# Kernel optimization log

Hardware: AMD Instinct MI355X
Metric: run time of the kernel (lower is better)

Reference implementation:

```python
import jax, jax.numpy as jnp
import numpy as np

N, E, D, R = 8192, 131072, 128, 32
SIZES = (3, 5, 7)  # per-degree component counts (2l+1)
LN_EPS = 1e-5


def setup_inputs() -> dict:
    key = jax.random.key(0)
    ks = jax.random.split(key, 20)
    rn = lambda k, shape, s=1.0: jax.random.normal(k, shape, jnp.float32) * s
    inp = {
        'X0': rn(ks[0], (N, SIZES[0], D)),
        'X1': rn(ks[1], (N, SIZES[1], D)),
        'X2': rn(ks[2], (N, SIZES[2], D)),
        't_ij': rn(ks[3], (E, D)),
        'r0': rn(ks[4], (E, SIZES[0])),
        'r1': rn(ks[5], (E, SIZES[1])),
        'r2': rn(ks[6], (E, SIZES[2])),
        'edge_index': jax.random.randint(ks[7], (2, E), 0, N, dtype=jnp.int32),
        # params
        'W_vq': rn(ks[8], (D, R), D ** -0.5),
        'W_vk0': rn(ks[9], (D, R), D ** -0.5),
        'W_vk1': rn(ks[10], (D, R), D ** -0.5),
        'W_vk2': rn(ks[11], (D, R), D ** -0.5),
        'ln_g': jnp.ones((R,), jnp.float32),
        'ln_b': jnp.zeros((R,), jnp.float32),
        'W_w': rn(ks[12], (R, D), R ** -0.5),
        'b_w': jnp.zeros((D,), jnp.float32),
        'W_t1': rn(ks[13], (D, D), D ** -0.5),
        'b_t1': jnp.zeros((D,), jnp.float32),
        'W_t2': rn(ks[14], (D, D), D ** -0.5),
        'b_t2': jnp.zeros((D,), jnp.float32),
    }
    return inp


def _vec_rej(x, r):
    # x: [E, L, R], r: [E, L]; dot over component dim (L), keepdim, subtract projection
    r = r[..., None]
    dot = jnp.sum(x * r, axis=1, keepdims=True)  # [E, 1, R]
    return x - dot * r


def reference(X0, X1, X2, t_ij, r0, r1, r2, edge_index,
              W_vq, W_vk0, W_vk1, W_vk2, ln_g, ln_b, W_w, b_w,
              W_t1, b_t1, W_t2, b_t2):
    n_j, n_i = edge_index[0], edge_index[1]
    X_ls = jnp.concatenate([X0, X1, X2], axis=1)                 # [N, 15, D]
    eq_i = jnp.einsum('nld,dr->nlr', X_ls, W_vq)[n_i]            # [E, 15, R]
    ek = jnp.concatenate([
        jnp.einsum('nld,dr->nlr', X0, W_vk0),
        jnp.einsum('nld,dr->nlr', X1, W_vk1),
        jnp.einsum('nld,dr->nlr', X2, W_vk2)], axis=1)
    ek_j = ek[n_j]                                               # [E, 15, R]
    # per-degree vector rejection (vec_rej=True)
    qs, ksl, off = [], [], 0
    for r in (r0, r1, r2):
        s = r.shape[1]
        qs.append(_vec_rej(eq_i[:, off:off + s], r))
        ksl.append(_vec_rej(ek_j[:, off:off + s], -r))
        off += s
    eq_i = jnp.concatenate(qs, axis=1)
    ek_j = jnp.concatenate(ksl, axis=1)
    w_ij = jnp.sum(eq_i * ek_j, axis=1)                          # [E, R]
    # mlp_w = LayerNorm + Linear
    mu = jnp.mean(w_ij, axis=-1, keepdims=True)
    var = jnp.var(w_ij, axis=-1, keepdims=True)
    wn = (w_ij - mu) * jax.lax.rsqrt(var + LN_EPS) * ln_g + ln_b
    dw = wn @ W_w + b_w                                          # [E, D]
    # mlp_t = Linear -> silu -> Linear, then outer activation
    t = jax.nn.silu(t_ij @ W_t1 + b_t1) @ W_t2 + b_t2            # [E, D]
    return dw * jax.nn.silu(t)
```

## Files before the change

kernel.cpp:

```cpp
#include <hip/hip_runtime.h>
#include <hip/hip_bf16.h>

#define N_NODES 8192
#define N_EDGES 131072
#define LN_EPS  1e-5f

typedef __attribute__((ext_vector_type(8))) short bf16x8;
typedef __attribute__((ext_vector_type(4))) short bf16x4;
typedef __attribute__((ext_vector_type(4))) float f32x4;

__device__ __forceinline__ float silu_f(float x) {
    return x * __builtin_amdgcn_rcpf(1.0f + __expf(-x));
}

__device__ __forceinline__ unsigned short f2bf(float x) {
    union { float f; unsigned int u; } v; v.f = x;
    unsigned int r = v.u + 0x7FFFu + ((v.u >> 16) & 1u);
    return (unsigned short)(r >> 16);
}
__device__ __forceinline__ float bf2f(unsigned short u) {
    union { float f; unsigned int x; } v; v.x = ((unsigned int)u) << 16;
    return v.f;
}
__device__ __forceinline__ unsigned int pk2(float a, float b) {
    float2 t; t.x = a; t.y = b;
    union { __hip_bfloat162 h; unsigned int u; } v;
    v.h = __float22bfloat162_rn(t);
    return v.u;
}
__device__ __forceinline__ bf16x8 pack8(float4 u, float4 v) {
    union { bf16x8 b; unsigned int w[4]; } o;
    o.w[0] = pk2(u.x, u.y); o.w[1] = pk2(u.z, u.w);
    o.w[2] = pk2(v.x, v.y); o.w[3] = pk2(v.z, v.w);
    return o.b;
}
__device__ __forceinline__ bf16x4 pack4(float a, float b, float c, float d) {
    union { bf16x4 v; unsigned int u[2]; } o;
    o.u[0] = pk2(a, b); o.u[1] = pk2(c, d);
    return o.v;
}
__device__ __forceinline__ f32x4 mfma16(bf16x8 a, bf16x8 b, f32x4 c) {
    return __builtin_amdgcn_mfma_f32_16x16x32_bf16(a, b, c, 0, 0, 0);
}
#if __has_builtin(__builtin_amdgcn_mfma_f32_16x16x16bf16_1k)
__device__ __forceinline__ f32x4 mfma_k16(bf16x4 a, bf16x4 b, f32x4 c) {
    return __builtin_amdgcn_mfma_f32_16x16x16bf16_1k(a, b, c, 0, 0, 0);
}
#else
__device__ __forceinline__ f32x4 mfma_k16(bf16x4 a, bf16x4 b, f32x4 c) {
    f32x4 d;
    asm("v_mfma_f32_16x16x16_bf16 %0, %1, %2, %3"
        : "=v"(d) : "v"(a), "v"(b), "v"(c));
    return d;
}
#endif

__global__ __launch_bounds__(256) void prep_kernel(
    const float* __restrict__ W_w, const float* __restrict__ W_t1,
    const float* __restrict__ W_t2, const float* __restrict__ Wvq,
    const float* __restrict__ Wvk0, const float* __restrict__ Wvk1,
    const float* __restrict__ Wvk2,
    unsigned short* __restrict__ Wtw, unsigned short* __restrict__ Wt1b,
    unsigned short* __restrict__ Wt2b, unsigned short* __restrict__ Wqt,
    unsigned short* __restrict__ Wk0t, unsigned short* __restrict__ Wk1t,
    unsigned short* __restrict__ Wk2t)
{
    int i = blockIdx.x * 256 + threadIdx.x;
    if (i < 16384) {
        int n = i >> 7, k = i & 127;
        Wt1b[i] = f2bf(W_t1[k * 128 + n]);
        Wt2b[i] = f2bf(W_t2[k * 128 + n]);
    }
    if (i < 4096) {
        { int n = i >> 5, k = i & 31; Wtw[i] = f2bf(W_w[k * 128 + n]); }
        int r = i >> 7, d = i & 127;
        Wqt[i]  = f2bf(Wvq [d * 32 + r]);
        Wk0t[i] = f2bf(Wvk0[d * 32 + r]);
        Wk1t[i] = f2bf(Wvk1[d * 32 + r]);
        Wk2t[i] = f2bf(Wvk2[d * 32 + r]);
    }
}

template<int S, int LOFF>
__device__ __forceinline__ void proj_body(
    const float* __restrict__ X, const unsigned short* __restrict__ Wqt,
    const unsigned short* __restrict__ Wkt,
    unsigned short* __restrict__ eq, unsigned short* __restrict__ ek,
    int row0)
{
    const int tid  = threadIdx.x;
    const int lane = tid & 63;
    const int wv   = tid >> 6;
    const int l15  = lane & 15;
    const int lk   = lane >> 4;
    const int xrow = row0 + wv * 16 + l15;

    bf16x8 xf[4];
    #pragma unroll
    for (int kt = 0; kt < 4; ++kt) {
        const float* p = X + (size_t)xrow * 128 + kt * 32 + lk * 8;
        xf[kt] = pack8(*(const float4*)p, *(const float4*)(p + 4));
    }

    f32x4 qa[2], ka[2];
    #pragma unroll
    for (int h = 0; h < 2; ++h) {
        qa[h] = (f32x4){0.f, 0.f, 0.f, 0.f};
        ka[h] = (f32x4){0.f, 0.f, 0.f, 0.f};
    }
    #pragma unroll
    for (int kt = 0; kt < 4; ++kt) {
        #pragma unroll
        for (int h = 0; h < 2; ++h) {
            bf16x8 wq = *(const bf16x8*)&Wqt[(h * 16 + l15) * 128 + kt * 32 + lk * 8];
            bf16x8 wk = *(const bf16x8*)&Wkt[(h * 16 + l15) * 128 + kt * 32 + lk * 8];
            qa[h] = mfma16(wq, xf[kt], qa[h]);
            ka[h] = mfma16(wk, xf[kt], ka[h]);
        }
    }

    const int n = xrow / S;
    const int l = xrow % S + LOFF;
    const size_t base = (size_t)n * 512 + l;
    #pragma unroll
    for (int h = 0; h < 2; ++h) {
        #pragma unroll
        for (int j = 0; j < 4; ++j) {
            const int r = h * 16 + lk * 4 + j;
            eq[base + r * 16] = f2bf(qa[h][j]);
            ek[base + r * 16] = f2bf(ka[h][j]);
        }
    }
}

__global__ __launch_bounds__(256) void proj_kernel(
    const float* __restrict__ X0, const float* __restrict__ X1,
    const float* __restrict__ X2,
    const unsigned short* __restrict__ Wqt,
    const unsigned short* __restrict__ Wk0t,
    const unsigned short* __restrict__ Wk1t,
    const unsigned short* __restrict__ Wk2t,
    unsigned short* __restrict__ eq, unsigned short* __restrict__ ek)
{
    const int b = blockIdx.x;
    if (b < 384)
        proj_body<3, 0>(X0, Wqt, Wk0t, eq, ek, b * 64);
    else if (b < 1024)
        proj_body<5, 3>(X1, Wqt, Wk1t, eq, ek, (b - 384) * 64);
    else
        proj_body<7, 8>(X2, Wqt, Wk2t, eq, ek, (b - 1024) * 64);
}

__device__ __forceinline__ float edge_w(
    bf16x8 q0, bf16x8 q1, bf16x8 k0, bf16x8 k1, const float* rv)
{
    float qv[15], kv[15];
    #pragma unroll
    for (int l = 0; l < 8; ++l) {
        qv[l] = bf2f((unsigned short)q0[l]);
        kv[l] = bf2f((unsigned short)k0[l]);
    }
    #pragma unroll
    for (int l = 8; l < 15; ++l) {
        qv[l] = bf2f((unsigned short)q1[l - 8]);
        kv[l] = bf2f((unsigned short)k1[l - 8]);
    }
    float qk = 0.f;
    #pragma unroll
    for (int l = 0; l < 15; ++l) qk = fmaf(qv[l], kv[l], qk);
    float c0 = 2.f, c1 = 2.f, c2 = 2.f;
    #pragma unroll
    for (int l = 0; l < 3; ++l)  c0 -= rv[l] * rv[l];
    #pragma unroll
    for (int l = 3; l < 8; ++l)  c1 -= rv[l] * rv[l];
    #pragma unroll
    for (int l = 8; l < 15; ++l) c2 -= rv[l] * rv[l];
    float dq0 = 0.f, dk0 = 0.f, dq1 = 0.f, dk1 = 0.f, dq2 = 0.f, dk2 = 0.f;
    #pragma unroll
    for (int l = 0; l < 3; ++l)  { dq0 = fmaf(qv[l], rv[l], dq0); dk0 = fmaf(kv[l], rv[l], dk0); }
    #pragma unroll
    for (int l = 3; l < 8; ++l)  { dq1 = fmaf(qv[l], rv[l], dq1); dk1 = fmaf(kv[l], rv[l], dk1); }
    #pragma unroll
    for (int l = 8; l < 15; ++l) { dq2 = fmaf(qv[l], rv[l], dq2); dk2 = fmaf(kv[l], rv[l], dk2); }
    return qk - dq0 * dk0 * c0 - dq1 * dk1 * c1 - dq2 * dk2 * c2;
}

__global__ __launch_bounds__(256) void wn_kernel(
    const unsigned short* __restrict__ eq, const unsigned short* __restrict__ ek,
    const float* __restrict__ r0, const float* __restrict__ r1,
    const float* __restrict__ r2, const int* __restrict__ eidx,
    const float* __restrict__ ln_g, const float* __restrict__ ln_b,
    unsigned short* __restrict__ wn)
{
    const int tid = threadIdx.x;
    const int r   = tid & 31;
    const int hw  = tid >> 5;
    const int e0  = blockIdx.x * 16 + hw * 2;
    const int e1  = e0 + 1;
    const float g  = ln_g[r];
    const float bb = ln_b[r];

    const int nj0 = eidx[e0], ni0 = eidx[N_EDGES + e0];
    const int nj1 = eidx[e1], ni1 = eidx[N_EDGES + e1];

    const unsigned short* qp0 = eq + (size_t)ni0 * 512 + r * 16;
    const unsigned short* kp0 = ek + (size_t)nj0 * 512 + r * 16;
    const unsigned short* qp1 = eq + (size_t)ni1 * 512 + r * 16;
    const unsigned short* kp1 = ek + (size_t)nj1 * 512 + r * 16;
    bf16x8 qa0 = *(const bf16x8*)qp0, qb0 = *(const bf16x8*)(qp0 + 8);
    bf16x8 ka0 = *(const bf16x8*)kp0, kb0 = *(const bf16x8*)(kp0 + 8);
    bf16x8 qa1 = *(const bf16x8*)qp1, qb1 = *(const bf16x8*)(qp1 + 8);
    bf16x8 ka1 = *(const bf16x8*)kp1, kb1 = *(const bf16x8*)(kp1 + 8);

    float rva[15], rvb[15];
    #pragma unroll
    for (int c = 0; c < 3; ++c) { rva[c]     = r0[e0 * 3 + c]; rvb[c]     = r0[e1 * 3 + c]; }
    #pragma unroll
    for (int c = 0; c < 5; ++c) { rva[3 + c] = r1[e0 * 5 + c]; rvb[3 + c] = r1[e1 * 5 + c]; }
    #pragma unroll
    for (int c = 0; c < 7; ++c) { rva[8 + c] = r2[e0 * 7 + c]; rvb[8 + c] = r2[e1 * 7 + c]; }

    const float w0 = edge_w(qa0, qb0, ka0, kb0, rva);
    const float w1 = edge_w(qa1, qb1, ka1, kb1, rvb);

    float s0 = w0, s20 = w0 * w0, s1 = w1, s21 = w1 * w1;
    #pragma unroll
    for (int off = 1; off < 32; off <<= 1) {
        s0  += __shfl_xor(s0,  off); s20 += __shfl_xor(s20, off);
        s1  += __shfl_xor(s1,  off); s21 += __shfl_xor(s21, off);
    }
    const float mu0   = s0 * (1.f / 32.f);
    const float var0  = s20 * (1.f / 32.f) - mu0 * mu0;
    const float mu1   = s1 * (1.f / 32.f);
    const float var1  = s21 * (1.f / 32.f) - mu1 * mu1;
    wn[(size_t)e0 * 32 + r] = f2bf((w0 - mu0) * rsqrtf(var0 + LN_EPS) * g + bb);
    wn[(size_t)e1 * 32 + r] = f2bf((w1 - mu1) * rsqrtf(var1 + LN_EPS) * g + bb);
}

__global__ __launch_bounds__(256) void edge_kernel(
    const float* __restrict__ t_ij,
    const unsigned short* __restrict__ wn,
    const unsigned short* __restrict__ Wtw, const float* __restrict__ b_w,
    const unsigned short* __restrict__ Wt1, const float* __restrict__ b_t1,
    const unsigned short* __restrict__ Wt2, const float* __restrict__ b_t2,
    float* __restrict__ out)
{
    const int tid  = threadIdx.x;
    const int lane = tid & 63;
    const int wv   = tid >> 6;
    const int l15  = lane & 15;
    const int lk   = lane >> 4;
    const int tile = (blockIdx.x * 4 + wv) * 64;

    bf16x8 a1[4][4];
    #pragma unroll
    for (int kt = 0; kt < 4; ++kt)
        #pragma unroll
        for (int rt = 0; rt < 4; ++rt) {
            const float* p = t_ij + (size_t)(tile + rt * 16 + l15) * 128
                           + kt * 32 + lk * 8;
            a1[kt][rt] = pack8(*(const float4*)p, *(const float4*)(p + 4));
        }

    bf16x8 wnf[4];
    #pragma unroll
    for (int rt = 0; rt < 4; ++rt)
        wnf[rt] = *(const bf16x8*)&wn[(size_t)(tile + rt * 16 + l15) * 32 + lk * 8];

    bf16x4 h[4][8];
    #pragma unroll
    for (int ct = 0; ct < 8; ++ct) {
        bf16x8 w1f[4];
        #pragma unroll
        for (int kt = 0; kt < 4; ++kt)
            w1f[kt] = *(const bf16x8*)&Wt1[(size_t)(ct * 16 + l15) * 128
                                           + kt * 32 + lk * 8];
        f32x4 ac[4];
        #pragma unroll
        for (int rt = 0; rt < 4; ++rt) ac[rt] = (f32x4){0.f, 0.f, 0.f, 0.f};
        #pragma unroll
        for (int kt = 0; kt < 4; ++kt)
            #pragma unroll
            for (int rt = 0; rt < 4; ++rt)
                ac[rt] = mfma16(w1f[kt], a1[kt][rt], ac[rt]);

        const float4 bt1 = *(const float4*)&b_t1[ct * 16 + lk * 4];
        #pragma unroll
        for (int rt = 0; rt < 4; ++rt)
            h[rt][ct] = pack4(silu_f(ac[rt][0] + bt1.x),
                              silu_f(ac[rt][1] + bt1.y),
                              silu_f(ac[rt][2] + bt1.z),
                              silu_f(ac[rt][3] + bt1.w));
    }

    #pragma unroll
    for (int ct2 = 0; ct2 < 8; ++ct2) {
        bf16x4 w2b[8];
        #pragma unroll
        for (int ct1 = 0; ct1 < 8; ++ct1)
            w2b[ct1] = *(const bf16x4*)&Wt2[(size_t)(ct2 * 16 + l15) * 128
                                            + ct1 * 16 + lk * 4];
        bf16x8 wwf = *(const bf16x8*)&Wtw[(ct2 * 16 + l15) * 32 + lk * 8];
        const float bwv = b_w[ct2 * 16 + l15];
        const float b2v = b_t2[ct2 * 16 + l15];

        #pragma unroll
        for (int rt = 0; rt < 4; ++rt) {
            f32x4 o = (f32x4){0.f, 0.f, 0.f, 0.f};
            #pragma unroll
            for (int ct1 = 0; ct1 < 8; ++ct1)
                o = mfma_k16(h[rt][ct1], w2b[ct1], o);
            f32x4 d = mfma16(wnf[rt], wwf, (f32x4){0.f, 0.f, 0.f, 0.f});

            float* op = out + (size_t)(tile + rt * 16 + lk * 4) * 128
                      + ct2 * 16 + l15;
            #pragma unroll
            for (int j = 0; j < 4; ++j)
                op[j * 128] = (d[j] + bwv) * silu_f(o[j] + b2v);
        }
    }
}

extern "C" void kernel_launch(void* const* d_in, const int* in_sizes, int n_in,
                              void* d_out, int out_size, void* d_ws, size_t ws_size,
                              hipStream_t stream) {
    (void)in_sizes; (void)n_in; (void)out_size; (void)ws_size;
    const float* X0   = (const float*)d_in[0];
    const float* X1   = (const float*)d_in[1];
    const float* X2   = (const float*)d_in[2];
    const float* t_ij = (const float*)d_in[3];
    const float* r0   = (const float*)d_in[4];
    const float* r1   = (const float*)d_in[5];
    const float* r2   = (const float*)d_in[6];
    const int*   eidx = (const int*)d_in[7];
    const float* Wvq  = (const float*)d_in[8];
    const float* Wvk0 = (const float*)d_in[9];
    const float* Wvk1 = (const float*)d_in[10];
    const float* Wvk2 = (const float*)d_in[11];
    const float* ln_g = (const float*)d_in[12];
    const float* ln_b = (const float*)d_in[13];
    const float* W_w  = (const float*)d_in[14];
    const float* b_w  = (const float*)d_in[15];
    const float* W_t1 = (const float*)d_in[16];
    const float* b_t1 = (const float*)d_in[17];
    const float* W_t2 = (const float*)d_in[18];
    const float* b_t2 = (const float*)d_in[19];
    float* out = (float*)d_out;

    unsigned short* eq   = (unsigned short*)d_ws;
    unsigned short* ek   = eq  + (size_t)N_NODES * 512;
    unsigned short* wn   = ek  + (size_t)N_NODES * 512;
    unsigned short* Wtw  = wn  + (size_t)N_EDGES * 32;
    unsigned short* Wt1b = Wtw  + 4096;
    unsigned short* Wt2b = Wt1b + 16384;
    unsigned short* Wqt  = Wt2b + 16384;
    unsigned short* Wk0t = Wqt  + 4096;
    unsigned short* Wk1t = Wk0t + 4096;
    unsigned short* Wk2t = Wk1t + 4096;

    prep_kernel<<<64, 256, 0, stream>>>(W_w, W_t1, W_t2, Wvq, Wvk0, Wvk1, Wvk2,
                                        Wtw, Wt1b, Wt2b, Wqt, Wk0t, Wk1t, Wk2t);
    proj_kernel<<<1920, 256, 0, stream>>>(X0, X1, X2, Wqt, Wk0t, Wk1t, Wk2t,
                                          eq, ek);
    wn_kernel<<<N_EDGES / 16, 256, 0, stream>>>(eq, ek, r0, r1, r2, eidx,
                                                ln_g, ln_b, wn);
    edge_kernel<<<N_EDGES / 256, 256, 0, stream>>>(t_ij, wn, Wtw, b_w,
                                                   Wt1b, b_t1, Wt2b, b_t2, out);
}
```

Measured before the change: 115.2 us.

## Restructure projection per node with LDS transpose; halve edge tile per wave

The projection kernel now gives each wave one node and covers all 15 component rows (padded to 16) in a single MFMA tile. It computes all three key projections and selects per row, then transposes through LDS so eq/ek are written with 16-byte vector stores instead of scattered 2-byte stores. The edge kernel processes 32 edges per wave instead of 64 and launches twice as many blocks, which lowers register pressure and may raise occupancy. The cost is redundant key MFMAs, one wasted padded row, and more reloads of the edge-kernel weights.

```diff
diff --git a/kernel.cpp b/kernel.cpp
--- a/kernel.cpp
+++ b/kernel.cpp
@@ -81,58 +81,6 @@
     }
 }
 
-template<int S, int LOFF>
-__device__ __forceinline__ void proj_body(
-    const float* __restrict__ X, const unsigned short* __restrict__ Wqt,
-    const unsigned short* __restrict__ Wkt,
-    unsigned short* __restrict__ eq, unsigned short* __restrict__ ek,
-    int row0)
-{
-    const int tid  = threadIdx.x;
-    const int lane = tid & 63;
-    const int wv   = tid >> 6;
-    const int l15  = lane & 15;
-    const int lk   = lane >> 4;
-    const int xrow = row0 + wv * 16 + l15;
-
-    bf16x8 xf[4];
-    #pragma unroll
-    for (int kt = 0; kt < 4; ++kt) {
-        const float* p = X + (size_t)xrow * 128 + kt * 32 + lk * 8;
-        xf[kt] = pack8(*(const float4*)p, *(const float4*)(p + 4));
-    }
-
-    f32x4 qa[2], ka[2];
-    #pragma unroll
-    for (int h = 0; h < 2; ++h) {
-        qa[h] = (f32x4){0.f, 0.f, 0.f, 0.f};
-        ka[h] = (f32x4){0.f, 0.f, 0.f, 0.f};
-    }
-    #pragma unroll
-    for (int kt = 0; kt < 4; ++kt) {
-        #pragma unroll
-        for (int h = 0; h < 2; ++h) {
-            bf16x8 wq = *(const bf16x8*)&Wqt[(h * 16 + l15) * 128 + kt * 32 + lk * 8];
-            bf16x8 wk = *(const bf16x8*)&Wkt[(h * 16 + l15) * 128 + kt * 32 + lk * 8];
-            qa[h] = mfma16(wq, xf[kt], qa[h]);
-            ka[h] = mfma16(wk, xf[kt], ka[h]);
-        }
-    }
-
-    const int n = xrow / S;
-    const int l = xrow % S + LOFF;
-    const size_t base = (size_t)n * 512 + l;
-    #pragma unroll
-    for (int h = 0; h < 2; ++h) {
-        #pragma unroll
-        for (int j = 0; j < 4; ++j) {
-            const int r = h * 16 + lk * 4 + j;
-            eq[base + r * 16] = f2bf(qa[h][j]);
-            ek[base + r * 16] = f2bf(ka[h][j]);
-        }
-    }
-}
-
 __global__ __launch_bounds__(256) void proj_kernel(
     const float* __restrict__ X0, const float* __restrict__ X1,
     const float* __restrict__ X2,
@@ -142,13 +90,69 @@
     const unsigned short* __restrict__ Wk2t,
     unsigned short* __restrict__ eq, unsigned short* __restrict__ ek)
 {
-    const int b = blockIdx.x;
-    if (b < 384)
-        proj_body<3, 0>(X0, Wqt, Wk0t, eq, ek, b * 64);
-    else if (b < 1024)
-        proj_body<5, 3>(X1, Wqt, Wk1t, eq, ek, (b - 384) * 64);
-    else
-        proj_body<7, 8>(X2, Wqt, Wk2t, eq, ek, (b - 1024) * 64);
+    __shared__ __align__(16) unsigned short Tq[4][32][16];
+    __shared__ __align__(16) unsigned short Tk[4][32][16];
+
+    const int tid  = threadIdx.x;
+    const int lane = tid & 63;
+    const int wv   = tid >> 6;
+    const int l15  = lane & 15;
+    const int lk   = lane >> 4;
+    const int node = blockIdx.x * 4 + wv;
+    const int l    = (l15 < 14) ? l15 : 14;
+
+    const float* xsrc;
+    if (l < 3)      xsrc = X0 + ((size_t)node * 3 + l)       * 128;
+    else if (l < 8) xsrc = X1 + ((size_t)node * 5 + (l - 3)) * 128;
+    else            xsrc = X2 + ((size_t)node * 7 + (l - 8)) * 128;
+
+    bf16x8 xf[4];
+    #pragma unroll
+    for (int kt = 0; kt < 4; ++kt) {
+        const float* p = xsrc + kt * 32 + lk * 8;
+        xf[kt] = pack8(*(const float4*)p, *(const float4*)(p + 4));
+    }
+
+    f32x4 qa[2], k0a[2], k1a[2], k2a[2];
+    #pragma unroll
+    for (int h = 0; h < 2; ++h) {
+        qa[h]  = (f32x4){0.f, 0.f, 0.f, 0.f};
+        k0a[h] = (f32x4){0.f, 0.f, 0.f, 0.f};
+        k1a[h] = (f32x4){0.f, 0.f, 0.f, 0.f};
+        k2a[h] = (f32x4){0.f, 0.f, 0.f, 0.f};
+    }
+    #pragma unroll
+    for (int kt = 0; kt < 4; ++kt) {
+        #pragma unroll
+        for (int h = 0; h < 2; ++h) {
+            const size_t wo = (size_t)(h * 16 + l15) * 128 + kt * 32 + lk * 8;
+            qa[h]  = mfma16(*(const bf16x8*)&Wqt [wo], xf[kt], qa[h]);
+            k0a[h] = mfma16(*(const bf16x8*)&Wk0t[wo], xf[kt], k0a[h]);
+            k1a[h] = mfma16(*(const bf16x8*)&Wk1t[wo], xf[kt], k1a[h]);
+            k2a[h] = mfma16(*(const bf16x8*)&Wk2t[wo], xf[kt], k2a[h]);
+        }
+    }
+
+    #pragma unroll
+    for (int h = 0; h < 2; ++h) {
+        f32x4 ka = (l15 < 3) ? k0a[h] : ((l15 < 8) ? k1a[h] : k2a[h]);
+        #pragma unroll
+        for (int j = 0; j < 4; ++j) {
+            const int r = h * 16 + lk * 4 + j;
+            Tq[wv][r][l15] = f2bf(qa[h][j]);
+            Tk[wv][r][l15] = f2bf(ka[j]);
+        }
+    }
+    asm volatile("s_waitcnt lgkmcnt(0)" ::: "memory");
+    __builtin_amdgcn_sched_barrier(0);
+
+    const int r    = lane >> 1;
+    const int half = lane & 1;
+    bf16x8 vq = *(const bf16x8*)&Tq[wv][r][half * 8];
+    bf16x8 vk = *(const bf16x8*)&Tk[wv][r][half * 8];
+    const size_t base = (size_t)node * 512 + r * 16 + half * 8;
+    *(bf16x8*)&eq[base] = vq;
+    *(bf16x8*)&ek[base] = vk;
 }
 
 __device__ __forceinline__ float edge_w(
@@ -250,24 +254,24 @@
     const int wv   = tid >> 6;
     const int l15  = lane & 15;
     const int lk   = lane >> 4;
-    const int tile = (blockIdx.x * 4 + wv) * 64;
-
-    bf16x8 a1[4][4];
+    const int tile = (blockIdx.x * 4 + wv) * 32;
+
+    bf16x8 a1[4][2];
     #pragma unroll
     for (int kt = 0; kt < 4; ++kt)
         #pragma unroll
-        for (int rt = 0; rt < 4; ++rt) {
+        for (int rt = 0; rt < 2; ++rt) {
             const float* p = t_ij + (size_t)(tile + rt * 16 + l15) * 128
                            + kt * 32 + lk * 8;
             a1[kt][rt] = pack8(*(const float4*)p, *(const float4*)(p + 4));
         }
 
-    bf16x8 wnf[4];
-    #pragma unroll
-    for (int rt = 0; rt < 4; ++rt)
+    bf16x8 wnf[2];
+    #pragma unroll
+    for (int rt = 0; rt < 2; ++rt)
         wnf[rt] = *(const bf16x8*)&wn[(size_t)(tile + rt * 16 + l15) * 32 + lk * 8];
 
-    bf16x4 h[4][8];
+    bf16x4 h[2][8];
     #pragma unroll
     for (int ct = 0; ct < 8; ++ct) {
         bf16x8 w1f[4];
@@ -275,18 +279,18 @@
         for (int kt = 0; kt < 4; ++kt)
             w1f[kt] = *(const bf16x8*)&Wt1[(size_t)(ct * 16 + l15) * 128
                                            + kt * 32 + lk * 8];
-        f32x4 ac[4];
-        #pragma unroll
-        for (int rt = 0; rt < 4; ++rt) ac[rt] = (f32x4){0.f, 0.f, 0.f, 0.f};
+        f32x4 ac[2];
+        #pragma unroll
+        for (int rt = 0; rt < 2; ++rt) ac[rt] = (f32x4){0.f, 0.f, 0.f, 0.f};
         #pragma unroll
         for (int kt = 0; kt < 4; ++kt)
             #pragma unroll
-            for (int rt = 0; rt < 4; ++rt)
+            for (int rt = 0; rt < 2; ++rt)
                 ac[rt] = mfma16(w1f[kt], a1[kt][rt], ac[rt]);
 
         const float4 bt1 = *(const float4*)&b_t1[ct * 16 + lk * 4];
         #pragma unroll
-        for (int rt = 0; rt < 4; ++rt)
+        for (int rt = 0; rt < 2; ++rt)
             h[rt][ct] = pack4(silu_f(ac[rt][0] + bt1.x),
                               silu_f(ac[rt][1] + bt1.y),
                               silu_f(ac[rt][2] + bt1.z),
@@ -305,7 +309,7 @@
         const float b2v = b_t2[ct2 * 16 + l15];
 
         #pragma unroll
-        for (int rt = 0; rt < 4; ++rt) {
+        for (int rt = 0; rt < 2; ++rt) {
             f32x4 o = (f32x4){0.f, 0.f, 0.f, 0.f};
             #pragma unroll
             for (int ct1 = 0; ct1 < 8; ++ct1)
@@ -360,10 +364,10 @@
 
     prep_kernel<<<64, 256, 0, stream>>>(W_w, W_t1, W_t2, Wvq, Wvk0, Wvk1, Wvk2,
                                         Wtw, Wt1b, Wt2b, Wqt, Wk0t, Wk1t, Wk2t);
-    proj_kernel<<<1920, 256, 0, stream>>>(X0, X1, X2, Wqt, Wk0t, Wk1t, Wk2t,
-                                          eq, ek);
+    proj_kernel<<<N_NODES / 4, 256, 0, stream>>>(X0, X1, X2,
+                                                 Wqt, Wk0t, Wk1t, Wk2t, eq, ek);
     wn_kernel<<<N_EDGES / 16, 256, 0, stream>>>(eq, ek, r0, r1, r2, eidx,
                                                 ln_g, ln_b, wn);
-    edge_kernel<<<N_EDGES / 256, 256, 0, stream>>>(t_ij, wn, Wtw, b_w,
+    edge_kernel<<<N_EDGES / 128, 256, 0, stream>>>(t_ij, wn, Wtw, b_w,
                                                    Wt1b, b_t1, Wt2b, b_t2, out);
 }
```

Measured after the change: 138.0 us. 1.2x slower.
